# Kernel tuning notes

Measured on AMD Instinct MI355X. Metric: run time of the kernel, lower is better.

## Reference

```python
import jax, jax.numpy as jnp
import numpy as np

DIM = 1024
HID = 256
MAXT = 2048
B = 4
T = 2048


def setup_inputs() -> dict:
    key = jax.random.key(0)
    ks = jax.random.split(key, 10)
    s_in = 1.0 / np.sqrt(DIM)   # keeps K ~ N(0,1) so exp(K) is stable
    s_h = 1.0 / np.sqrt(HID)
    # xavier-uniform bound for square wbias: sqrt(6/(T+T))
    wb_bound = float(np.sqrt(6.0 / (MAXT + MAXT)))
    return {
        "x": jax.random.normal(ks[0], (B, T, DIM), dtype=jnp.float32),
        "Wq": jax.random.normal(ks[1], (DIM, HID), dtype=jnp.float32) * s_in,
        "bq": jnp.zeros((HID,), dtype=jnp.float32),
        "Wk": jax.random.normal(ks[2], (DIM, HID), dtype=jnp.float32) * s_in,
        "bk": jnp.zeros((HID,), dtype=jnp.float32),
        "Wv": jax.random.normal(ks[3], (DIM, HID), dtype=jnp.float32) * s_in,
        "bv": jnp.zeros((HID,), dtype=jnp.float32),
        "Wp": jax.random.normal(ks[4], (HID, DIM), dtype=jnp.float32) * s_h,
        "bp": jnp.zeros((DIM,), dtype=jnp.float32),
        "wbias": jax.random.uniform(ks[5], (MAXT, MAXT), dtype=jnp.float32,
                                    minval=-wb_bound, maxval=wb_bound),
    }


def reference(x, Wq, bq, Wk, bk, Wv, bv, Wp, bp, wbias):
    Bn, Tn, _ = x.shape
    Q = x @ Wq + bq            # [B,T,H]
    K = x @ Wk + bk            # [B,T,H]
    V = x @ Wv + bv            # [B,T,H]
    ew = jnp.exp(wbias[:Tn, :Tn])          # [T,T]
    eK = jnp.exp(K)                         # [B,T,H]
    num = jnp.einsum('ts,bsh->bth', ew, eK * V)   # [B,T,H]
    den = jnp.einsum('ts,bsh->bth', ew, eK)       # [B,T,H]
    Yt = jax.nn.sigmoid(Q) * (num / den)          # [B,T,H]
    return Yt @ Wp + bp                            # [B,T,DIM]
```

## Files before the change

### kernel.cpp

```cpp
#include <hip/hip_runtime.h>
#include <hip/hip_bf16.h>


#define T_   2048
#define DIM_ 1024
#define HID_ 256
#define B_   4

typedef __attribute__((ext_vector_type(8))) short bf16x8;
typedef __attribute__((ext_vector_type(4))) float f32x4;

static __device__ __forceinline__ unsigned short f2b(float f) {
  __hip_bfloat16 h = __float2bfloat16(f);
  return __builtin_bit_cast(unsigned short, h);
}

static __device__ __forceinline__ void gld16(const void* g, const void* l) {
  __builtin_amdgcn_global_load_lds((const __attribute__((address_space(1))) void*)g,
                                   (__attribute__((address_space(3))) void*)l, 16, 0, 0);
}

template <int BN>
__global__ __launch_bounds__(256) void gemm_bt(
    const unsigned short* __restrict__ A,
    const unsigned short* __restrict__ Bt,
    float* __restrict__ C,
    const float* __restrict__ bias,
    int M, int N, int K, int Ksub)
{
  __shared__ unsigned short As[128 * 32];
  __shared__ unsigned short Bs[BN * 32];
  const int tid  = threadIdx.x;
  const int lane = tid & 63;
  const int wave = tid >> 6;
  const int wr = wave >> 1, wc = wave & 1;
  const long bm = (long)blockIdx.y * 128;
  const long bn = (long)blockIdx.x * BN;
  const long kbase = (long)blockIdx.z * Ksub;

  const int srow = tid >> 2;
  const int sk   = (tid & 3) * 8;
  const unsigned short* ap0 = A  + (bm + srow) * (long)K + kbase + sk;
  const unsigned short* ap1 = ap0 + 64 * (long)K;
  const unsigned short* bp0 = Bt + (bn + srow) * (long)K + kbase + sk;
  const unsigned short* bp1 = bp0 + 64 * (long)K;

  char* AsB = (char*)As;
  char* BsB = (char*)Bs;
  char* ldsA0 = AsB + wave * 1024;
  char* ldsA1 = AsB + 4096 + wave * 1024;
  char* ldsB0 = BsB + wave * 1024;
  char* ldsB1 = BsB + 4096 + wave * 1024;

  constexpr int NF = BN / 32;
  f32x4 acc[4][NF] = {};

  const int fr  = lane & 15;
  const int fkb = (lane >> 4) * 16;

  const int nk = Ksub >> 5;
  for (int kt = 0; kt < nk; ++kt) {
    gld16(ap0, ldsA0);
    gld16(ap1, ldsA1);
    gld16(bp0, ldsB0);
    if constexpr (BN == 128) gld16(bp1, ldsB1);
    ap0 += 32; ap1 += 32; bp0 += 32;
    if constexpr (BN == 128) bp1 += 32;
    asm volatile("s_waitcnt vmcnt(0)" ::: "memory");
    __syncthreads();

    bf16x8 av[4], bv[NF];
#pragma unroll
    for (int m = 0; m < 4; ++m)
      av[m] = *(const bf16x8*)(AsB + (wr * 64 + m * 16 + fr) * 64 + fkb);
#pragma unroll
    for (int n = 0; n < NF; ++n)
      bv[n] = *(const bf16x8*)(BsB + (wc * (BN / 2) + n * 16 + fr) * 64 + fkb);
#pragma unroll
    for (int m = 0; m < 4; ++m)
#pragma unroll
      for (int n = 0; n < NF; ++n)
        acc[m][n] = __builtin_amdgcn_mfma_f32_16x16x32_bf16(av[m], bv[n], acc[m][n], 0, 0, 0);
    __syncthreads();
  }

  float* Cz = C + (long)blockIdx.z * M * (long)N;
  const long crow0 = bm + wr * 64 + ((lane >> 4) << 2);
  const long ccol0 = bn + wc * (BN / 2) + fr;
#pragma unroll
  for (int n = 0; n < NF; ++n) {
    const long col = ccol0 + n * 16;
    const float bb = bias ? bias[col] : 0.f;
#pragma unroll
    for (int m = 0; m < 4; ++m) {
#pragma unroll
      for (int r = 0; r < 4; ++r) {
        Cz[(crow0 + m * 16 + r) * (long)N + col] = acc[m][n][r] + bb;
      }
    }
  }
}

__global__ void prep_kernel(const float* __restrict__ x, const float* __restrict__ wbias,
                            const float* __restrict__ Wq, const float* __restrict__ Wk,
                            const float* __restrict__ Wv, const float* __restrict__ bq,
                            const float* __restrict__ bk, const float* __restrict__ bv,
                            const float* __restrict__ Wp,
                            unsigned short* __restrict__ xb, unsigned short* __restrict__ ewb,
                            unsigned short* __restrict__ WqkvT, unsigned short* __restrict__ WpT,
                            float* __restrict__ biascat) {
  const int bid = blockIdx.x;
  const int t = threadIdx.x;
  if (bid < 8192) {
    int i = bid * 256 + t;
    float4 v = ((const float4*)x)[i];
    ushort4 o; o.x = f2b(v.x); o.y = f2b(v.y); o.z = f2b(v.z); o.w = f2b(v.w);
    ((ushort4*)xb)[i] = o;
  } else if (bid < 12288) {
    int i = (bid - 8192) * 256 + t;
    float4 v = ((const float4*)wbias)[i];
    ushort4 o;
    o.x = f2b(__expf(v.x)); o.y = f2b(__expf(v.y));
    o.z = f2b(__expf(v.z)); o.w = f2b(__expf(v.w));
    ((ushort4*)ewb)[i] = o;
  } else {
    int idx = (bid - 12288) * 256 + t;
    if (idx < 768 * 1024) {
      int n = idx >> 10, k = idx & 1023;
      const float* W = (n < 256) ? Wq : (n < 512) ? Wk : Wv;
      WqkvT[idx] = f2b(W[k * 256 + (n & 255)]);
    }
    if (idx < 1024 * 256) {
      int d = idx >> 8, h = idx & 255;
      WpT[idx] = f2b(Wp[h * 1024 + d]);
    }
    if (idx < 768) {
      const float* bb = (idx < 256) ? bq : (idx < 512) ? bk : bv;
      biascat[idx] = bb[idx & 255];
    }
  }
}

__global__ void elt1_kernel(const float* __restrict__ C1, unsigned short* __restrict__ B2T) {
  __shared__ unsigned short ekT[64][65];
  __shared__ unsigned short ekvT[64][65];
  const int h0 = blockIdx.x * 64;
  const int s0 = blockIdx.y * 64;
  const int b  = blockIdx.z;
  const int t  = threadIdx.x;
#pragma unroll
  for (int i = 0; i < 16; ++i) {
    int idx = i * 256 + t;
    int si = idx >> 6, hi = idx & 63;
    const float* base = C1 + (long)(b * T_ + s0 + si) * 768;
    float k = base[256 + h0 + hi];
    float v = base[512 + h0 + hi];
    float ek = __expf(k);
    ekT[hi][si]  = f2b(ek);
    ekvT[hi][si] = f2b(ek * v);
  }
  __syncthreads();
#pragma unroll
  for (int i = 0; i < 16; ++i) {
    int idx = i * 256 + t;
    int hi = idx >> 6, si = idx & 63;
    B2T[(long)(b * 512 + h0 + hi) * 2048 + s0 + si]       = ekvT[hi][si];
    B2T[(long)(b * 512 + 256 + h0 + hi) * 2048 + s0 + si] = ekT[hi][si];
  }
}

__global__ void elt2_kernel(const float* __restrict__ C1, const float* __restrict__ C2,
                            unsigned short* __restrict__ Yt, int nslices) {
  int idx = blockIdx.x * 256 + threadIdx.x;
  int h = idx & 255, m = idx >> 8;
  int b = m >> 11, tt = m & 2047;
  long i_num = (long)tt * 2048 + b * 512 + h;
  long i_den = i_num + 256;
  float q   = C1[(long)m * 768 + h];
  float num = C2[i_num];
  float den = C2[i_den];
  if (nslices == 2) {
    num += C2[i_num + 4194304];
    den += C2[i_den + 4194304];
  }
  float sig = 1.f / (1.f + __expf(-q));
  Yt[idx] = f2b(sig * num / den);
}

extern "C" void kernel_launch(void* const* d_in, const int* in_sizes, int n_in,
                              void* d_out, int out_size, void* d_ws, size_t ws_size,
                              hipStream_t stream) {
  const float* x     = (const float*)d_in[0];
  const float* Wq    = (const float*)d_in[1];
  const float* bq    = (const float*)d_in[2];
  const float* Wk    = (const float*)d_in[3];
  const float* bk    = (const float*)d_in[4];
  const float* Wv    = (const float*)d_in[5];
  const float* bv    = (const float*)d_in[6];
  const float* Wp    = (const float*)d_in[7];
  const float* bp    = (const float*)d_in[8];
  const float* wbias = (const float*)d_in[9];

  char* ws = (char*)d_ws;
  const bool big = ws_size >= 76021760ull;

  unsigned short *xb, *WqkvT, *WpT, *ewb, *Yt, *B2T;
  float *C1, *C2, *biascat;
  if (big) {
    xb      = (unsigned short*)(ws + 0);
    WqkvT   = (unsigned short*)(ws + 16777216);
    biascat = (float*)(ws + 18350080);
    C2      = (float*)(ws + 0);
    ewb     = (unsigned short*)(ws + 33554432);
    Yt      = (unsigned short*)(ws + 33554432);
    C1      = (float*)(ws + 41943040);
    B2T     = (unsigned short*)(ws + 67108864);
    WpT     = (unsigned short*)(ws + 75497472);
  } else {
    xb      = (unsigned short*)(ws + 0);
    C2      = (float*)(ws + 0);
    WqkvT   = (unsigned short*)(ws + 16777216);
    WpT     = (unsigned short*)(ws + 18350080);
    biascat = (float*)(ws + 18874368);
    ewb     = (unsigned short*)(ws + 18878464);
    Yt      = (unsigned short*)(ws + 18878464);
    C1      = (float*)(ws + 27267072);
    B2T     = (unsigned short*)(ws + 52432896);
  }
  float* out = (float*)d_out;

  prep_kernel<<<15360, 256, 0, stream>>>(x, wbias, Wq, Wk, Wv, bq, bk, bv, Wp,
                                         xb, ewb, WqkvT, WpT, biascat);

  gemm_bt<64><<<dim3(12, 64, 1), 256, 0, stream>>>(xb, WqkvT, C1, biascat, 8192, 768, 1024, 1024);
  elt1_kernel<<<dim3(4, 32, 4), 256, 0, stream>>>(C1, B2T);
  if (big) {
    gemm_bt<128><<<dim3(16, 16, 2), 256, 0, stream>>>(ewb, B2T, C2, nullptr, 2048, 2048, 2048, 1024);
  } else {
    gemm_bt<64><<<dim3(32, 16, 1), 256, 0, stream>>>(ewb, B2T, C2, nullptr, 2048, 2048, 2048, 2048);
  }
  elt2_kernel<<<8192, 256, 0, stream>>>(C1, C2, Yt, big ? 2 : 1);
  gemm_bt<64><<<dim3(16, 64, 1), 256, 0, stream>>>(Yt, WpT, out, bp, 8192, 1024, 256, 256);
}
```

Before: 201.1 us.

## Fuse elementwise stages into GEMM epilogues and double-buffer LDS loads

```diff
diff --git a/kernel.cpp b/kernel.cpp
--- a/kernel.cpp
+++ b/kernel.cpp
@@ -1,11 +1,6 @@
 #include <hip/hip_runtime.h>
 #include <hip/hip_bf16.h>
 
-
-#define T_   2048
-#define DIM_ 1024
-#define HID_ 256
-#define B_   4
 
 typedef __attribute__((ext_vector_type(8))) short bf16x8;
 typedef __attribute__((ext_vector_type(4))) float f32x4;
@@ -20,84 +15,194 @@
                                    (__attribute__((address_space(3))) void*)l, 16, 0, 0);
 }
 
-template <int BN>
-__global__ __launch_bounds__(256) void gemm_bt(
-    const unsigned short* __restrict__ A,
-    const unsigned short* __restrict__ Bt,
-    float* __restrict__ C,
-    const float* __restrict__ bias,
-    int M, int N, int K, int Ksub)
-{
-  __shared__ unsigned short As[128 * 32];
-  __shared__ unsigned short Bs[BN * 32];
-  const int tid  = threadIdx.x;
-  const int lane = tid & 63;
-  const int wave = tid >> 6;
-  const int wr = wave >> 1, wc = wave & 1;
-  const long bm = (long)blockIdx.y * 128;
-  const long bn = (long)blockIdx.x * BN;
-  const long kbase = (long)blockIdx.z * Ksub;
-
+static __device__ __forceinline__ void gemm_loop(
+    const unsigned short* __restrict__ A_blk,
+    const unsigned short* __restrict__ Bt_blk,
+    int K, int nk, char* AsB, char* BsB, f32x4 acc[4][2],
+    int tid, int wr, int wc, int fr, int fkb)
+{
   const int srow = tid >> 2;
   const int sk   = (tid & 3) * 8;
-  const unsigned short* ap0 = A  + (bm + srow) * (long)K + kbase + sk;
+  const unsigned short* ap0 = A_blk + (long)srow * K + sk;
   const unsigned short* ap1 = ap0 + 64 * (long)K;
-  const unsigned short* bp0 = Bt + (bn + srow) * (long)K + kbase + sk;
-  const unsigned short* bp1 = bp0 + 64 * (long)K;
-
-  char* AsB = (char*)As;
-  char* BsB = (char*)Bs;
-  char* ldsA0 = AsB + wave * 1024;
-  char* ldsA1 = AsB + 4096 + wave * 1024;
-  char* ldsB0 = BsB + wave * 1024;
-  char* ldsB1 = BsB + 4096 + wave * 1024;
-
-  constexpr int NF = BN / 32;
-  f32x4 acc[4][NF] = {};
-
-  const int fr  = lane & 15;
-  const int fkb = (lane >> 4) * 16;
-
-  const int nk = Ksub >> 5;
+  const unsigned short* bp0 = Bt_blk + (long)srow * K + sk;
+
+  gld16(ap0, AsB + tid * 16);
+  gld16(ap1, AsB + 4096 + tid * 16);
+  gld16(bp0, BsB + tid * 16);
+  ap0 += 32; ap1 += 32; bp0 += 32;
+  __syncthreads();
+
+  int buf = 0;
   for (int kt = 0; kt < nk; ++kt) {
-    gld16(ap0, ldsA0);
-    gld16(ap1, ldsA1);
-    gld16(bp0, ldsB0);
-    if constexpr (BN == 128) gld16(bp1, ldsB1);
-    ap0 += 32; ap1 += 32; bp0 += 32;
-    if constexpr (BN == 128) bp1 += 32;
-    asm volatile("s_waitcnt vmcnt(0)" ::: "memory");
-    __syncthreads();
-
-    bf16x8 av[4], bv[NF];
+    if (kt + 1 < nk) {
+      char* nA = AsB + ((buf ^ 1) << 13) + tid * 16;
+      char* nB = BsB + ((buf ^ 1) << 12) + tid * 16;
+      gld16(ap0, nA);
+      gld16(ap1, nA + 4096);
+      gld16(bp0, nB);
+      ap0 += 32; ap1 += 32; bp0 += 32;
+    }
+    const char* Ab = AsB + (buf << 13);
+    const char* Bb = BsB + (buf << 12);
+    bf16x8 av[4], bv[2];
 #pragma unroll
     for (int m = 0; m < 4; ++m)
-      av[m] = *(const bf16x8*)(AsB + (wr * 64 + m * 16 + fr) * 64 + fkb);
-#pragma unroll
-    for (int n = 0; n < NF; ++n)
-      bv[n] = *(const bf16x8*)(BsB + (wc * (BN / 2) + n * 16 + fr) * 64 + fkb);
+      av[m] = *(const bf16x8*)(Ab + (wr * 64 + m * 16 + fr) * 64 + fkb);
+#pragma unroll
+    for (int n = 0; n < 2; ++n)
+      bv[n] = *(const bf16x8*)(Bb + (wc * 32 + n * 16 + fr) * 64 + fkb);
 #pragma unroll
     for (int m = 0; m < 4; ++m)
 #pragma unroll
-      for (int n = 0; n < NF; ++n)
+      for (int n = 0; n < 2; ++n)
         acc[m][n] = __builtin_amdgcn_mfma_f32_16x16x32_bf16(av[m], bv[n], acc[m][n], 0, 0, 0);
     __syncthreads();
-  }
-
-  float* Cz = C + (long)blockIdx.z * M * (long)N;
-  const long crow0 = bm + wr * 64 + ((lane >> 4) << 2);
-  const long ccol0 = bn + wc * (BN / 2) + fr;
-#pragma unroll
-  for (int n = 0; n < NF; ++n) {
+    buf ^= 1;
+  }
+}
+
+__global__ __launch_bounds__(256) void gemm1_qkv(
+    const unsigned short* __restrict__ xb, const unsigned short* __restrict__ WqkvT,
+    const float* __restrict__ biascat,
+    float* __restrict__ sgQ, unsigned short* __restrict__ B2T)
+{
+  __shared__ char AsB[16384];
+  __shared__ char BsB[8192];
+  const int tid = threadIdx.x, lane = tid & 63, wave = tid >> 6;
+  const int wr = wave >> 1, wc = wave & 1;
+  const int fr = lane & 15, fkb = (lane >> 4) * 16, q4 = (lane >> 4) * 2 * 2;
+  const long bm = (long)blockIdx.y * 128;
+  const long bn = (long)blockIdx.x * 64;
+  const int  b  = (int)(bm >> 11);
+  const int  tb = (int)(bm & 2047);
+
+  f32x4 acc[4][2] = {};
+  gemm_loop(xb + bm * 1024, WqkvT + bn * 1024, 1024, 32, AsB, BsB, acc,
+            tid, wr, wc, fr, fkb);
+
+  if (bn < 256) {
+#pragma unroll
+    for (int n = 0; n < 2; ++n) {
+      const int col = (int)bn + wc * 32 + n * 16 + fr;
+      const float bb = biascat[col];
+#pragma unroll
+      for (int m = 0; m < 4; ++m) {
+#pragma unroll
+        for (int r = 0; r < 4; ++r) {
+          long row = bm + wr * 64 + m * 16 + q4 + r;
+          float v = acc[m][n][r] + bb;
+          sgQ[row * 256 + col] = 1.f / (1.f + __expf(-v));
+        }
+      }
+    }
+  } else {
+#pragma unroll
+    for (int n = 0; n < 2; ++n) {
+      const int col = (int)bn + wc * 32 + n * 16 + fr;
+      const int u   = col - 256;
+      const float bb = biascat[col];
+      const bool isK = (u & 1) == 0;
+      const long rw = (long)b * 512 + u + (isK ? 1 : -1);
+#pragma unroll
+      for (int m = 0; m < 4; ++m) {
+        float v[4], o[4];
+#pragma unroll
+        for (int r = 0; r < 4; ++r) v[r] = acc[m][n][r] + bb;
+#pragma unroll
+        for (int r = 0; r < 4; ++r) o[r] = __shfl_xor(v[r], 1);
+        ushort4 pk;
+        if (isK) {
+          pk.x = f2b(__expf(v[0])); pk.y = f2b(__expf(v[1]));
+          pk.z = f2b(__expf(v[2])); pk.w = f2b(__expf(v[3]));
+        } else {
+          pk.x = f2b(__expf(o[0]) * v[0]); pk.y = f2b(__expf(o[1]) * v[1]);
+          pk.z = f2b(__expf(o[2]) * v[2]); pk.w = f2b(__expf(o[3]) * v[3]);
+        }
+        const int t0 = tb + wr * 64 + m * 16 + q4;
+        *(ushort4*)(B2T + rw * 2048 + t0) = pk;
+      }
+    }
+  }
+}
+
+__global__ __launch_bounds__(256) void gemm2_aft(
+    const unsigned short* __restrict__ ewb, const unsigned short* __restrict__ B2T,
+    const float* __restrict__ sgQ, unsigned short* __restrict__ Yt)
+{
+  __shared__ char AsB[16384];
+  __shared__ char BsB[8192];
+  __shared__ float epi[128 * 32];
+  const int tid = threadIdx.x, lane = tid & 63, wave = tid >> 6;
+  const int wr = wave >> 1, wc = wave & 1;
+  const int fr = lane & 15, fkb = (lane >> 4) * 16, q4 = (lane >> 4) * 2 * 2;
+  const long bm = (long)blockIdx.y * 128;
+  const long bn = (long)blockIdx.x * 64;
+  const int  b  = (int)(bn >> 9);
+  const int  h0 = (int)((bn & 511) >> 1);
+
+  f32x4 acc[4][2] = {};
+  gemm_loop(ewb + bm * 2048, B2T + bn * 2048, 2048, 64, AsB, BsB, acc,
+            tid, wr, wc, fr, fkb);
+
+  const bool even = (fr & 1) == 0;
+#pragma unroll
+  for (int n = 0; n < 2; ++n) {
+    const int hl = wc * 16 + n * 8 + (fr >> 1);
+#pragma unroll
+    for (int m = 0; m < 4; ++m) {
+#pragma unroll
+      for (int r = 0; r < 4; ++r) {
+        float own = acc[m][n][r];
+        float oth = __shfl_xor(own, 1);
+        if (even) {
+          int tl = wr * 64 + m * 16 + q4 + r;
+          epi[tl * 32 + hl] = own / oth;
+        }
+      }
+    }
+  }
+  __syncthreads();
+
+  const long mbase = (long)b * 2048 + bm;
+#pragma unroll
+  for (int p = 0; p < 16; ++p) {
+    int row = p * 8 + (tid >> 5);
+    int hl  = tid & 31;
+    long mrow = mbase + row;
+    int  hg   = h0 + hl;
+    float v = epi[row * 32 + hl] * sgQ[mrow * 256 + hg];
+    Yt[mrow * 256 + hg] = f2b(v);
+  }
+}
+
+__global__ __launch_bounds__(256) void gemm_bt(
+    const unsigned short* __restrict__ A, const unsigned short* __restrict__ Bt,
+    float* __restrict__ C, const float* __restrict__ bias, int M, int N, int K)
+{
+  __shared__ char AsB[16384];
+  __shared__ char BsB[8192];
+  const int tid = threadIdx.x, lane = tid & 63, wave = tid >> 6;
+  const int wr = wave >> 1, wc = wave & 1;
+  const int fr = lane & 15, fkb = (lane >> 4) * 16, q4 = (lane >> 4) * 2 * 2;
+  const long bm = (long)blockIdx.y * 128;
+  const long bn = (long)blockIdx.x * 64;
+
+  f32x4 acc[4][2] = {};
+  gemm_loop(A + bm * (long)K, Bt + bn * (long)K, K, K >> 5, AsB, BsB, acc,
+            tid, wr, wc, fr, fkb);
+
+  const long crow0 = bm + wr * 64 + q4;
+  const long ccol0 = bn + wc * 32 + fr;
+#pragma unroll
+  for (int n = 0; n < 2; ++n) {
     const long col = ccol0 + n * 16;
     const float bb = bias ? bias[col] : 0.f;
 #pragma unroll
-    for (int m = 0; m < 4; ++m) {
-#pragma unroll
-      for (int r = 0; r < 4; ++r) {
-        Cz[(crow0 + m * 16 + r) * (long)N + col] = acc[m][n][r] + bb;
-      }
-    }
+    for (int m = 0; m < 4; ++m)
+#pragma unroll
+      for (int r = 0; r < 4; ++r)
+        C[(crow0 + m * 16 + r) * (long)N + col] = acc[m][n][r] + bb;
   }
 }
 
@@ -127,64 +232,22 @@
     int idx = (bid - 12288) * 256 + t;
     if (idx < 768 * 1024) {
       int n = idx >> 10, k = idx & 1023;
-      const float* W = (n < 256) ? Wq : (n < 512) ? Wk : Wv;
-      WqkvT[idx] = f2b(W[k * 256 + (n & 255)]);
+      const float* W; int c;
+      if (n < 256) { W = Wq; c = n; }
+      else { int u = n - 256; c = u >> 1; W = (u & 1) ? Wv : Wk; }
+      WqkvT[idx] = f2b(W[k * 256 + c]);
     }
     if (idx < 1024 * 256) {
       int d = idx >> 8, h = idx & 255;
       WpT[idx] = f2b(Wp[h * 1024 + d]);
     }
     if (idx < 768) {
-      const float* bb = (idx < 256) ? bq : (idx < 512) ? bk : bv;
-      biascat[idx] = bb[idx & 255];
-    }
-  }
-}
-
-__global__ void elt1_kernel(const float* __restrict__ C1, unsigned short* __restrict__ B2T) {
-  __shared__ unsigned short ekT[64][65];
-  __shared__ unsigned short ekvT[64][65];
-  const int h0 = blockIdx.x * 64;
-  const int s0 = blockIdx.y * 64;
-  const int b  = blockIdx.z;
-  const int t  = threadIdx.x;
-#pragma unroll
-  for (int i = 0; i < 16; ++i) {
-    int idx = i * 256 + t;
-    int si = idx >> 6, hi = idx & 63;
-    const float* base = C1 + (long)(b * T_ + s0 + si) * 768;
-    float k = base[256 + h0 + hi];
-    float v = base[512 + h0 + hi];
-    float ek = __expf(k);
-    ekT[hi][si]  = f2b(ek);
-    ekvT[hi][si] = f2b(ek * v);
-  }
-  __syncthreads();
-#pragma unroll
-  for (int i = 0; i < 16; ++i) {
-    int idx = i * 256 + t;
-    int hi = idx >> 6, si = idx & 63;
-    B2T[(long)(b * 512 + h0 + hi) * 2048 + s0 + si]       = ekvT[hi][si];
-    B2T[(long)(b * 512 + 256 + h0 + hi) * 2048 + s0 + si] = ekT[hi][si];
-  }
-}
-
-__global__ void elt2_kernel(const float* __restrict__ C1, const float* __restrict__ C2,
-                            unsigned short* __restrict__ Yt, int nslices) {
-  int idx = blockIdx.x * 256 + threadIdx.x;
-  int h = idx & 255, m = idx >> 8;
-  int b = m >> 11, tt = m & 2047;
-  long i_num = (long)tt * 2048 + b * 512 + h;
-  long i_den = i_num + 256;
-  float q   = C1[(long)m * 768 + h];
-  float num = C2[i_num];
-  float den = C2[i_den];
-  if (nslices == 2) {
-    num += C2[i_num + 4194304];
-    den += C2[i_den + 4194304];
-  }
-  float sig = 1.f / (1.f + __expf(-q));
-  Yt[idx] = f2b(sig * num / den);
+      float v;
+      if (idx < 256) v = bq[idx];
+      else { int u = idx - 256; v = (u & 1) ? bv[u >> 1] : bk[u >> 1]; }
+      biascat[idx] = v;
+    }
+  }
 }
 
 extern "C" void kernel_launch(void* const* d_in, const int* in_sizes, int n_in,
@@ -202,43 +265,19 @@
   const float* wbias = (const float*)d_in[9];
 
   char* ws = (char*)d_ws;
-  const bool big = ws_size >= 76021760ull;
-
-  unsigned short *xb, *WqkvT, *WpT, *ewb, *Yt, *B2T;
-  float *C1, *C2, *biascat;
-  if (big) {
-    xb      = (unsigned short*)(ws + 0);
-    WqkvT   = (unsigned short*)(ws + 16777216);
-    biascat = (float*)(ws + 18350080);
-    C2      = (float*)(ws + 0);
-    ewb     = (unsigned short*)(ws + 33554432);
-    Yt      = (unsigned short*)(ws + 33554432);
-    C1      = (float*)(ws + 41943040);
-    B2T     = (unsigned short*)(ws + 67108864);
-    WpT     = (unsigned short*)(ws + 75497472);
-  } else {
-    xb      = (unsigned short*)(ws + 0);
-    C2      = (float*)(ws + 0);
-    WqkvT   = (unsigned short*)(ws + 16777216);
-    WpT     = (unsigned short*)(ws + 18350080);
-    biascat = (float*)(ws + 18874368);
-    ewb     = (unsigned short*)(ws + 18878464);
-    Yt      = (unsigned short*)(ws + 18878464);
-    C1      = (float*)(ws + 27267072);
-    B2T     = (unsigned short*)(ws + 52432896);
-  }
+  unsigned short* xb      = (unsigned short*)(ws + 0);
+  unsigned short* ewb     = (unsigned short*)(ws + 16777216);
+  unsigned short* WqkvT   = (unsigned short*)(ws + 25165824);
+  unsigned short* WpT     = (unsigned short*)(ws + 26738688);
+  float*          biascat = (float*)(ws + 27262976);
+  float*          sgQ     = (float*)(ws + 27267072);
+  unsigned short* B2T     = (unsigned short*)(ws + 35655680);
+  unsigned short* Yt      = (unsigned short*)(ws + 44044288);
   float* out = (float*)d_out;
 
   prep_kernel<<<15360, 256, 0, stream>>>(x, wbias, Wq, Wk, Wv, bq, bk, bv, Wp,
                                          xb, ewb, WqkvT, WpT, biascat);
-
-  gemm_bt<64><<<dim3(12, 64, 1), 256, 0, stream>>>(xb, WqkvT, C1, biascat, 8192, 768, 1024, 1024);
-  elt1_kernel<<<dim3(4, 32, 4), 256, 0, stream>>>(C1, B2T);
-  if (big) {
-    gemm_bt<128><<<dim3(16, 16, 2), 256, 0, stream>>>(ewb, B2T, C2, nullptr, 2048, 2048, 2048, 1024);
-  } else {
-    gemm_bt<64><<<dim3(32, 16, 1), 256, 0, stream>>>(ewb, B2T, C2, nullptr, 2048, 2048, 2048, 2048);
-  }
-  elt2_kernel<<<8192, 256, 0, stream>>>(C1, C2, Yt, big ? 2 : 1);
-  gemm_bt<64><<<dim3(16, 64, 1), 256, 0, stream>>>(Yt, WpT, out, bp, 8192, 1024, 256, 256);
-}
+  gemm1_qkv<<<dim3(12, 64), 256, 0, stream>>>(xb, WqkvT, biascat, sgQ, B2T);
+  gemm2_aft<<<dim3(32, 16), 256, 0, stream>>>(ewb, B2T, sgQ, Yt);
+  gemm_bt<<<dim3(16, 64), 256, 0, stream>>>(Yt, WpT, out, bp, 8192, 1024, 256);
+}
```

Result: no change. 199.8 us (-0.6%).
